# Kernel tuning notes

Hardware: AMD Instinct MI355X
Metric: run time of the kernel (lower is better)

The kernel has to match this reference:

```python
import jax, jax.numpy as jnp
import numpy as np

N_HEAD = 16
HEAD_DIM = 64

def setup_inputs() -> dict:
    key = jax.random.key(0)
    k1, k2, k3 = jax.random.split(key, 3)
    B, S, D = 4, 2048, 1024
    x = jax.random.normal(k1, (B, S, D), dtype=jnp.float32)
    mask = jnp.tril(jnp.ones((S, S), dtype=bool))[None, None]  # (1,1,S,S) causal
    w_attn = jax.random.normal(k2, (D, 3 * D), dtype=jnp.float32) * (1.0 / np.sqrt(D))
    b_attn = jnp.zeros((3 * D,), dtype=jnp.float32)
    w_proj = jax.random.normal(k3, (D, D), dtype=jnp.float32) * (1.0 / np.sqrt(D))
    b_proj = jnp.zeros((D,), dtype=jnp.float32)
    return {"x": x, "mask": mask, "w_attn": w_attn, "b_attn": b_attn,
            "w_proj": w_proj, "b_proj": b_proj}

def reference(x, mask, w_attn, b_attn, w_proj, b_proj):
    B, S, D = x.shape
    H, hd = N_HEAD, HEAD_DIM
    qkv = x @ w_attn + b_attn                      # (B,S,3D)
    q, k, v = jnp.split(qkv, 3, axis=-1)
    q = q.reshape(B, S, H, hd).transpose(0, 2, 1, 3)  # (B,H,S,hd)
    k = k.reshape(B, S, H, hd).transpose(0, 2, 1, 3)
    v = v.reshape(B, S, H, hd).transpose(0, 2, 1, 3)
    scores = jnp.einsum('bhqd,bhkd->bhqk', q, k) / jnp.sqrt(jnp.float32(hd))
    scores = jnp.where(mask, scores, jnp.float32(-1e10))
    weights = jax.nn.softmax(scores, axis=-1)      # dropout is identity (deterministic=True)
    attn = jnp.einsum('bhqk,bhkd->bhqd', weights, v)
    attn = attn.transpose(0, 2, 1, 3).reshape(B, S, D)
    return attn @ w_proj + b_proj
```

## Files before the change

### kernel.cpp

```cpp
#include <hip/hip_runtime.h>
#include <hip/hip_bf16.h>
#include <stdint.h>


typedef uint16_t u16;
typedef __bf16 bf16x8 __attribute__((ext_vector_type(8)));
typedef __bf16 bf16x4 __attribute__((ext_vector_type(4)));
typedef short s16x4 __attribute__((ext_vector_type(4)));
typedef float f32x4 __attribute__((ext_vector_type(4)));

#define S_LEN 2048
#define DMODEL 1024
#define NHEAD 16
#define HDIM 64
#define MTOT 8192
#define NQKV 3072

__device__ __forceinline__ u16 f2bf(float f) {
    union { float f; uint32_t u; } v; v.f = f;
    uint32_t u = v.u;
    return (u16)((u + 0x7fffu + ((u >> 16) & 1u)) >> 16);
}

__device__ __forceinline__ s16x4 bits4(bf16x4 v) {
    union { bf16x4 b; s16x4 s; } u; u.b = v; return u.s;
}

__device__ __forceinline__ f32x4 mfma16(bf16x4 a, bf16x4 b, f32x4 c) {
    return __builtin_amdgcn_mfma_f32_16x16x16bf16_1k(bits4(a), bits4(b), c, 0, 0, 0);
}

__device__ __forceinline__ void async_load16(const void* g, void* l) {
    __builtin_amdgcn_global_load_lds(
        (__attribute__((address_space(1))) void*)g,
        (__attribute__((address_space(3))) void*)l,
        16, 0, 0);
}

__global__ void convert_x_kernel(const float4* __restrict__ in, ushort4* __restrict__ out, int n4) {
    int i = blockIdx.x * 256 + threadIdx.x;
    if (i < n4) {
        float4 f = in[i];
        ushort4 o;
        o.x = f2bf(f.x); o.y = f2bf(f.y); o.z = f2bf(f.z); o.w = f2bf(f.w);
        out[i] = o;
    }
}

__global__ void transpose_bf16_kernel(const float* __restrict__ in, u16* __restrict__ out, int R, int C) {
    __shared__ float tile[64][65];
    int r0 = blockIdx.y * 64, c0 = blockIdx.x * 64;
    #pragma unroll
    for (int i = 0; i < 16; ++i) {
        int idx = threadIdx.x + i * 256;
        int r = idx >> 6, c = idx & 63;
        tile[r][c] = in[(size_t)(r0 + r) * C + c0 + c];
    }
    __syncthreads();
    #pragma unroll
    for (int i = 0; i < 16; ++i) {
        int idx = threadIdx.x + i * 256;
        int c = idx >> 6, r = idx & 63;
        out[(size_t)(c0 + c) * R + r0 + r] = f2bf(tile[r][c]);
    }
}

__global__ void transpose_v_kernel(const u16* __restrict__ qkv, u16* __restrict__ vt) {
    __shared__ u16 tile[64 * 66];
    const int tid = threadIdx.x;
    const int stile = blockIdx.x, bh = blockIdx.y;
    const int b = bh >> 4, h = bh & 15;
    const u16* src = qkv + ((size_t)b * S_LEN + stile * 64) * NQKV + 2 * DMODEL + h * HDIM;
    #pragma unroll
    for (int it = 0; it < 2; ++it) {
        int item = it * 256 + tid;
        int s = item >> 3, d0 = (item & 7) * 8;
        bf16x8 v = *(const bf16x8*)(src + (size_t)s * NQKV + d0);
        const u16* vu = (const u16*)&v;
        #pragma unroll
        for (int j = 0; j < 8; ++j) tile[(d0 + j) * 66 + s] = vu[j];
    }
    __syncthreads();
    #pragma unroll
    for (int it = 0; it < 2; ++it) {
        int item = it * 256 + tid;
        int d = item >> 3, s0 = (item & 7) * 8;
        union { u16 u[8]; uint4 v; } pk;
        #pragma unroll
        for (int j = 0; j < 8; ++j) pk.u[j] = tile[d * 66 + s0 + j];
        *(uint4*)(vt + ((size_t)bh * 64 + d) * S_LEN + stile * 64 + s0) = pk.v;
    }
}

template<int NF, bool OUT_BF16>
__global__ __launch_bounds__(512, 2) void gemm16q(
    const u16* __restrict__ A, const u16* __restrict__ Bt,
    const float* __restrict__ bias, void* __restrict__ C,
    int M, int N, int K)
{
    constexpr int NBH = NF / 2;
    constexpr int BSLOT = NF * 4096;
    __shared__ __attribute__((aligned(16))) u16 sm[32768 + 2 * BSLOT];
    u16* const As = sm;
    u16* const Bs = sm + 32768;

    const int tid = threadIdx.x;
    const int wave = tid >> 6, lane = tid & 63;
    const int l15 = lane & 15, q4 = lane >> 4;
    const int wm = wave >> 2, wn = wave & 3;

    const int bid = (int)blockIdx.x;
    const int xcd = bid & 7;
    const int lx  = bid >> 3;
    const int MB  = M >> 8;
    const int PM  = MB >> 3;
    const int nb  = lx / PM;
    const int mb  = xcd * PM + (lx - nb * PM);
    const int m0 = mb << 8, n0 = nb * NF * 64;

    const u16* Ag = A + (size_t)m0 * K;
    const u16* Bg = Bt + (size_t)n0 * K;

    const int srow = tid >> 3;
    const size_t goff0 = (size_t)srow * K + (size_t)(((tid & 7) ^ (srow & 7)) * 8);
    const size_t goff1 = goff0 + (size_t)64 * K;
    const int ldso = tid * 8;

    const int ck0 = (q4 ^ (l15 & 7)) * 8;
    const int ck1 = ((4 + q4) ^ (l15 & 7)) * 8;
    const int rb0 = (wn * NF * 16 + l15) * 64;

    f32x4 acc[8][NF] = {};
    const int T = K >> 6;

#define STAGE_A(t_, h_) do { \
    const u16* ga_ = Ag + (size_t)(h_) * 128 * K + (size_t)(t_) * 64; \
    u16* da_ = As + (((t_) & 1) * 2 + (h_)) * 8192; \
    async_load16(ga_ + goff0, da_ + ldso); \
    async_load16(ga_ + goff1, da_ + ldso + 4096); \
} while (0)

#define STAGE_B(t_, h_) do { \
    const u16* gb_ = Bg + (size_t)(h_) * 128 * K + (size_t)(t_) * 64; \
    u16* db_ = Bs + ((t_) & 1) * BSLOT + (h_) * 8192; \
    async_load16(gb_ + goff0, db_ + ldso); \
    async_load16(gb_ + goff1, db_ + ldso + 4096); \
} while (0)

#define LOAD_AF(P_) do { \
    af[0][0] = *(const bf16x8*)(Ah + ((2 * (P_)) * 16 + l15) * 64 + ck0); \
    af[0][1] = *(const bf16x8*)(Ah + ((2 * (P_)) * 16 + l15) * 64 + ck1); \
    af[1][0] = *(const bf16x8*)(Ah + ((2 * (P_) + 1) * 16 + l15) * 64 + ck0); \
    af[1][1] = *(const bf16x8*)(Ah + ((2 * (P_) + 1) * 16 + l15) * 64 + ck1); \
} while (0)

#define PHASE_MFMA(P_) do { \
    __builtin_amdgcn_s_barrier(); \
    __builtin_amdgcn_s_setprio(1); \
    _Pragma("unroll") \
    for (int i_ = 0; i_ < 2; ++i_) \
        _Pragma("unroll") \
        for (int nf_ = 0; nf_ < NF; ++nf_) \
            _Pragma("unroll") \
            for (int kk_ = 0; kk_ < 2; ++kk_) \
                acc[2 * (P_) + i_][nf_] = __builtin_amdgcn_mfma_f32_16x16x32_bf16( \
                    af[i_][kk_], bfr[nf_][kk_], acc[2 * (P_) + i_][nf_], 0, 0, 0); \
    __builtin_amdgcn_s_setprio(0); \
} while (0)

    STAGE_A(0, 0); STAGE_A(0, 1);
    STAGE_B(0, 0); if constexpr (NBH == 2) STAGE_B(0, 1);
    if (T > 1) {
        STAGE_B(1, 0); if constexpr (NBH == 2) STAGE_B(1, 1);
        if constexpr (NBH == 2) asm volatile("s_waitcnt vmcnt(4)");
        else                    asm volatile("s_waitcnt vmcnt(2)");
    } else {
        asm volatile("s_waitcnt vmcnt(0)");
    }
    __builtin_amdgcn_sched_barrier(0);
    __builtin_amdgcn_s_barrier();

    for (int t = 0; t < T; ++t) {
        const int par = t & 1;
        const u16* Ah = As + (par * 2 + wm) * 8192;
        const u16* Bl = Bs + par * BSLOT;

        bf16x8 af[2][2], bfr[NF][2];

        #pragma unroll
        for (int nf = 0; nf < NF; ++nf) {
            bfr[nf][0] = *(const bf16x8*)(Bl + rb0 + nf * (16 * 64) + ck0);
            bfr[nf][1] = *(const bf16x8*)(Bl + rb0 + nf * (16 * 64) + ck1);
        }
        LOAD_AF(0);
        if (t + 1 < T) STAGE_A(t + 1, 0);
        PHASE_MFMA(0);
        __builtin_amdgcn_s_barrier();

        LOAD_AF(1);
        if (t + 1 < T) STAGE_A(t + 1, 1);
        PHASE_MFMA(1);
        __builtin_amdgcn_s_barrier();

        LOAD_AF(2);
        if (t + 2 < T) STAGE_B(t + 2, 0);
        PHASE_MFMA(2);
        __builtin_amdgcn_s_barrier();

        LOAD_AF(3);
        if constexpr (NBH == 2) { if (t + 2 < T) STAGE_B(t + 2, 1); }
        PHASE_MFMA(3);
        if (t + 1 < T) {
            if (t + 2 < T) {
                if constexpr (NBH == 2) asm volatile("s_waitcnt vmcnt(4)");
                else                    asm volatile("s_waitcnt vmcnt(2)");
            } else {
                asm volatile("s_waitcnt vmcnt(0)");
            }
            __builtin_amdgcn_sched_barrier(0);
            __builtin_amdgcn_s_barrier();
        }
    }

#undef STAGE_A
#undef STAGE_B
#undef LOAD_AF
#undef PHASE_MFMA

    #pragma unroll
    for (int mf = 0; mf < 8; ++mf) {
        const int row = m0 + wm * 128 + mf * 16 + q4 * 4;
        #pragma unroll
        for (int nf = 0; nf < NF; ++nf) {
            const int col = n0 + wn * NF * 16 + nf * 16 + l15;
            const float bv = bias[col];
            #pragma unroll
            for (int r = 0; r < 4; ++r) {
                float v = acc[mf][nf][r] + bv;
                if (OUT_BF16) ((u16*)C)[(size_t)(row + r) * N + col] = f2bf(v);
                else          ((float*)C)[(size_t)(row + r) * N + col] = v;
            }
        }
    }
}

__device__ __forceinline__ void stage_tiles(
    const u16* __restrict__ qkv, const u16* __restrict__ vt,
    size_t base, int bh, int h, int w, int srow8, int schunk,
    int kt, u16* __restrict__ KsB, u16* __restrict__ VsB)
{
    #pragma unroll
    for (int q = 0; q < 2; ++q) {
        int rloc = w * 16 + q * 8 + srow8;
        int sc = ((schunk ^ (rloc & 7)) * 8);
        async_load16(qkv + (base + (size_t)kt * 64 + rloc) * (size_t)NQKV + DMODEL + h * HDIM + sc,
                     KsB + (w * 16 + q * 8) * 64);
        async_load16(vt + ((size_t)bh * 64 + rloc) * S_LEN + kt * 64 + sc,
                     VsB + (w * 16 + q * 8) * 64);
    }
}

__device__ __forceinline__ void attn_pass(
    int qt, const u16* __restrict__ qkv, const u16* __restrict__ vt,
    __bf16* __restrict__ outb, u16 (*Ks)[64 * 64], u16 (*Vs)[64 * 64],
    int w, int lane, int bh, int h, size_t base)
{
    const int l15 = lane & 15, q4 = lane >> 4;
    const int srow8 = lane >> 3, schunk = lane & 7;

    const float QSCALE = 0.125f * 1.44269504f;
    bf16x8 qf[2][2];
    #pragma unroll
    for (int mh = 0; mh < 2; ++mh) {
        int qrow = qt * 128 + mh * 64 + w * 16 + l15;
        #pragma unroll
        for (int kc = 0; kc < 2; ++kc) {
            bf16x8 raw = *(const bf16x8*)(qkv + (base + qrow) * (size_t)NQKV + h * HDIM + kc * 32 + q4 * 8);
            bf16x8 sc;
            #pragma unroll
            for (int j = 0; j < 8; ++j) sc[j] = (__bf16)((float)raw[j] * QSCALE);
            qf[mh][kc] = sc;
        }
    }

    bf16x4 ones4;
    #pragma unroll
    for (int j = 0; j < 4; ++j) ones4[j] = (__bf16)1.0f;

    f32x4 o0[4] = {}, o1[4] = {};
    f32x4 la0 = {}, la1 = {};

    const int ktlast = 2 * qt + 1;

    __syncthreads();
    stage_tiles(qkv, vt, base, bh, h, w, srow8, schunk, 0, Ks[0], Vs[0]);
    if (ktlast >= 1)
        stage_tiles(qkv, vt, base, bh, h, w, srow8, schunk, 1, Ks[1], Vs[1]);

    for (int kt = 0; kt <= 2 * qt; ++kt) {
        const int buf = kt % 3;
        __syncthreads();
        int pf = kt + 2;
        if (pf <= ktlast)
            stage_tiles(qkv, vt, base, bh, h, w, srow8, schunk, pf, Ks[pf % 3], Vs[pf % 3]);

        f32x4 st0[4] = {}, st1[4] = {};
        #pragma unroll
        for (int nt = 0; nt < 4; ++nt) {
            int n = nt * 16 + l15;
            #pragma unroll
            for (int kc = 0; kc < 2; ++kc) {
                int ch = (((kc * 4 + q4) ^ (n & 7)) * 8);
                bf16x8 kf = *(const bf16x8*)(&Ks[buf][n * 64 + ch]);
                st0[nt] = __builtin_amdgcn_mfma_f32_16x16x32_bf16(kf, qf[0][kc], st0[nt], 0, 0, 0);
                st1[nt] = __builtin_amdgcn_mfma_f32_16x16x32_bf16(kf, qf[1][kc], st1[nt], 0, 0, 0);
            }
        }

        if (kt == 2 * qt) {
            #pragma unroll
            for (int nt = 0; nt < 4; ++nt)
                #pragma unroll
                for (int r = 0; r < 4; ++r) {
                    int keyl = nt * 16 + q4 * 4 + r;
                    if (keyl > w * 16 + l15) st0[nt][r] = -1e30f;
                }
        }

        bf16x4 pb0[4], pb1[4];
        #pragma unroll
        for (int nt = 0; nt < 4; ++nt)
            #pragma unroll
            for (int r = 0; r < 4; ++r) {
                pb0[nt][r] = (__bf16)__builtin_amdgcn_exp2f(st0[nt][r]);
                pb1[nt][r] = (__bf16)__builtin_amdgcn_exp2f(st1[nt][r]);
            }

        #pragma unroll
        for (int nt = 0; nt < 4; ++nt) {
            #pragma unroll
            for (int mt = 0; mt < 4; ++mt) {
                int row = mt * 16 + l15;
                int ch = (nt * 2 + (q4 >> 1)) ^ (row & 7);
                bf16x4 vf = *(const bf16x4*)(&Vs[buf][row * 64 + ch * 8 + (q4 & 1) * 4]);
                o0[mt] = mfma16(vf, pb0[nt], o0[mt]);
                o1[mt] = mfma16(vf, pb1[nt], o1[mt]);
            }
            la0 = mfma16(ones4, pb0[nt], la0);
            la1 = mfma16(ones4, pb1[nt], la1);
        }
    }

    {
        const int buf = ktlast % 3;
        __syncthreads();

        f32x4 st1[4] = {};
        #pragma unroll
        for (int nt = 0; nt < 4; ++nt) {
            int n = nt * 16 + l15;
            #pragma unroll
            for (int kc = 0; kc < 2; ++kc) {
                int ch = (((kc * 4 + q4) ^ (n & 7)) * 8);
                bf16x8 kf = *(const bf16x8*)(&Ks[buf][n * 64 + ch]);
                st1[nt] = __builtin_amdgcn_mfma_f32_16x16x32_bf16(kf, qf[1][kc], st1[nt], 0, 0, 0);
            }
        }
        bf16x4 pb1[4];
        #pragma unroll
        for (int nt = 0; nt < 4; ++nt)
            #pragma unroll
            for (int r = 0; r < 4; ++r) {
                int keyl = nt * 16 + q4 * 4 + r;
                float s = (keyl > w * 16 + l15) ? -1e30f : st1[nt][r];
                pb1[nt][r] = (__bf16)__builtin_amdgcn_exp2f(s);
            }
        #pragma unroll
        for (int nt = 0; nt < 4; ++nt) {
            #pragma unroll
            for (int mt = 0; mt < 4; ++mt) {
                int row = mt * 16 + l15;
                int ch = (nt * 2 + (q4 >> 1)) ^ (row & 7);
                bf16x4 vf = *(const bf16x4*)(&Vs[buf][row * 64 + ch * 8 + (q4 & 1) * 4]);
                o1[mt] = mfma16(vf, pb1[nt], o1[mt]);
            }
            la1 = mfma16(ones4, pb1[nt], la1);
        }
    }

    float inv0 = 1.0f / la0[0], inv1 = 1.0f / la1[0];
    int row0 = qt * 128 + w * 16 + l15;
    int row1 = row0 + 64;
    #pragma unroll
    for (int mt = 0; mt < 4; ++mt) {
        union { __bf16 b[4]; ushort4 v; } p0, p1;
        #pragma unroll
        for (int r = 0; r < 4; ++r) {
            p0.b[r] = (__bf16)(o0[mt][r] * inv0);
            p1.b[r] = (__bf16)(o1[mt][r] * inv1);
        }
        int col = h * HDIM + mt * 16 + q4 * 4;
        *(ushort4*)(&outb[(base + row0) * (size_t)DMODEL + col]) = p0.v;
        *(ushort4*)(&outb[(base + row1) * (size_t)DMODEL + col]) = p1.v;
    }
}

__global__ __launch_bounds__(256, 3) void attn_kernel(
    const u16* __restrict__ qkv, const u16* __restrict__ vt, u16* __restrict__ out)
{
    __shared__ __attribute__((aligned(16))) u16 Ks[3][64 * 64];
    __shared__ __attribute__((aligned(16))) u16 Vs[3][64 * 64];

    const int tid = threadIdx.x;
    const int w = tid >> 6, lane = tid & 63;
    const int bh = blockIdx.y;
    const int b = bh >> 4, h = bh & 15;
    const size_t base = (size_t)b * S_LEN;
    const int NT = (int)gridDim.x * 2;

    attn_pass(NT - 1 - (int)blockIdx.x, qkv, vt, (__bf16*)out, Ks, Vs, w, lane, bh, h, base);
    attn_pass((int)blockIdx.x,          qkv, vt, (__bf16*)out, Ks, Vs, w, lane, bh, h, base);
}

extern "C" void kernel_launch(void* const* d_in, const int* in_sizes, int n_in,
                              void* d_out, int out_size, void* d_ws, size_t ws_size,
                              hipStream_t stream) {
    const float* x      = (const float*)d_in[0];
    const float* w_attn = (const float*)d_in[2];
    const float* b_attn = (const float*)d_in[3];
    const float* w_proj = (const float*)d_in[4];
    const float* b_proj = (const float*)d_in[5];

    u16* xb   = (u16*)d_ws;
    u16* wat  = xb  + (size_t)MTOT * DMODEL;
    u16* wpt  = wat + (size_t)NQKV * DMODEL;
    u16* qkv  = wpt + (size_t)DMODEL * DMODEL;
    u16* attn = qkv + (size_t)MTOT * NQKV;
    u16* vt   = xb;

    convert_x_kernel<<<(MTOT * DMODEL / 4 + 255) / 256, 256, 0, stream>>>(
        (const float4*)x, (ushort4*)xb, MTOT * DMODEL / 4);
    transpose_bf16_kernel<<<dim3(NQKV / 64, DMODEL / 64), 256, 0, stream>>>(w_attn, wat, DMODEL, NQKV);
    transpose_bf16_kernel<<<dim3(DMODEL / 64, DMODEL / 64), 256, 0, stream>>>(w_proj, wpt, DMODEL, DMODEL);

    gemm16q<4, true><<<dim3((MTOT / 256) * (NQKV / 256)), 512, 0, stream>>>(
        xb, wat, b_attn, (void*)qkv, MTOT, NQKV, DMODEL);

    transpose_v_kernel<<<dim3(S_LEN / 64, 4 * NHEAD), 256, 0, stream>>>(qkv, vt);

    attn_kernel<<<dim3(S_LEN / 256, 4 * NHEAD), 256, 0, stream>>>(qkv, vt, attn);

    gemm16q<2, false><<<dim3((MTOT / 256) * (DMODEL / 128)), 512, 0, stream>>>(
        attn, wpt, b_proj, d_out, MTOT, DMODEL, DMODEL);
}
```

Measured before the change: 270.0 us.

## Widen attention query tile to 256 rows per pass for K/V reuse

Each attention pass now handles four 64-row query groups (256 rows) instead of two, so every staged K/V tile feeds up to four query groups of MFMAs. Causal masking is applied per group on its diagonal tile, and groups past their diagonal are skipped. The separate tail block is folded into the main loop. The grid halves and launch bounds drop to one block per SM hint. This costs much higher register pressure, fewer blocks, and worse causal load balance in exchange for less K/V staging traffic.

```diff
diff --git a/kernel.cpp b/kernel.cpp
--- a/kernel.cpp
+++ b/kernel.cpp
@@ -269,17 +269,17 @@
     const int srow8 = lane >> 3, schunk = lane & 7;
 
     const float QSCALE = 0.125f * 1.44269504f;
-    bf16x8 qf[2][2];
-    #pragma unroll
-    for (int mh = 0; mh < 2; ++mh) {
-        int qrow = qt * 128 + mh * 64 + w * 16 + l15;
+    bf16x8 qf[4][2];
+    #pragma unroll
+    for (int g = 0; g < 4; ++g) {
+        int qrow = qt * 256 + g * 64 + w * 16 + l15;
         #pragma unroll
         for (int kc = 0; kc < 2; ++kc) {
             bf16x8 raw = *(const bf16x8*)(qkv + (base + qrow) * (size_t)NQKV + h * HDIM + kc * 32 + q4 * 8);
             bf16x8 sc;
             #pragma unroll
             for (int j = 0; j < 8; ++j) sc[j] = (__bf16)((float)raw[j] * QSCALE);
-            qf[mh][kc] = sc;
+            qf[g][kc] = sc;
         }
     }
 
@@ -287,24 +287,23 @@
     #pragma unroll
     for (int j = 0; j < 4; ++j) ones4[j] = (__bf16)1.0f;
 
-    f32x4 o0[4] = {}, o1[4] = {};
-    f32x4 la0 = {}, la1 = {};
-
-    const int ktlast = 2 * qt + 1;
+    f32x4 o[4][4] = {};
+    f32x4 la[4] = {};
+
+    const int ktlast = 4 * qt + 3;
 
     __syncthreads();
     stage_tiles(qkv, vt, base, bh, h, w, srow8, schunk, 0, Ks[0], Vs[0]);
-    if (ktlast >= 1)
-        stage_tiles(qkv, vt, base, bh, h, w, srow8, schunk, 1, Ks[1], Vs[1]);
-
-    for (int kt = 0; kt <= 2 * qt; ++kt) {
+    stage_tiles(qkv, vt, base, bh, h, w, srow8, schunk, 1, Ks[1], Vs[1]);
+
+    for (int kt = 0; kt <= ktlast; ++kt) {
         const int buf = kt % 3;
         __syncthreads();
         int pf = kt + 2;
         if (pf <= ktlast)
             stage_tiles(qkv, vt, base, bh, h, w, srow8, schunk, pf, Ks[pf % 3], Vs[pf % 3]);
 
-        f32x4 st0[4] = {}, st1[4] = {};
+        f32x4 st[4][4] = {};
         #pragma unroll
         for (int nt = 0; nt < 4; ++nt) {
             int n = nt * 16 + l15;
@@ -312,29 +311,31 @@
             for (int kc = 0; kc < 2; ++kc) {
                 int ch = (((kc * 4 + q4) ^ (n & 7)) * 8);
                 bf16x8 kf = *(const bf16x8*)(&Ks[buf][n * 64 + ch]);
-                st0[nt] = __builtin_amdgcn_mfma_f32_16x16x32_bf16(kf, qf[0][kc], st0[nt], 0, 0, 0);
-                st1[nt] = __builtin_amdgcn_mfma_f32_16x16x32_bf16(kf, qf[1][kc], st1[nt], 0, 0, 0);
+                #pragma unroll
+                for (int g = 0; g < 4; ++g)
+                    if (kt <= 4 * qt + g)
+                        st[g][nt] = __builtin_amdgcn_mfma_f32_16x16x32_bf16(
+                            kf, qf[g][kc], st[g][nt], 0, 0, 0);
             }
         }
 
-        if (kt == 2 * qt) {
+        bf16x4 pb[4][4];
+        #pragma unroll
+        for (int g = 0; g < 4; ++g) {
+            if (kt > 4 * qt + g) continue;
+            const bool diag = (kt == 4 * qt + g);
             #pragma unroll
             for (int nt = 0; nt < 4; ++nt)
                 #pragma unroll
                 for (int r = 0; r < 4; ++r) {
-                    int keyl = nt * 16 + q4 * 4 + r;
-                    if (keyl > w * 16 + l15) st0[nt][r] = -1e30f;
+                    float s = st[g][nt][r];
+                    if (diag) {
+                        int keyl = nt * 16 + q4 * 4 + r;
+                        if (keyl > w * 16 + l15) s = -1e30f;
+                    }
+                    pb[g][nt][r] = (__bf16)__builtin_amdgcn_exp2f(s);
                 }
         }
-
-        bf16x4 pb0[4], pb1[4];
-        #pragma unroll
-        for (int nt = 0; nt < 4; ++nt)
-            #pragma unroll
-            for (int r = 0; r < 4; ++r) {
-                pb0[nt][r] = (__bf16)__builtin_amdgcn_exp2f(st0[nt][r]);
-                pb1[nt][r] = (__bf16)__builtin_amdgcn_exp2f(st1[nt][r]);
-            }
 
         #pragma unroll
         for (int nt = 0; nt < 4; ++nt) {
@@ -343,69 +344,35 @@
                 int row = mt * 16 + l15;
                 int ch = (nt * 2 + (q4 >> 1)) ^ (row & 7);
                 bf16x4 vf = *(const bf16x4*)(&Vs[buf][row * 64 + ch * 8 + (q4 & 1) * 4]);
-                o0[mt] = mfma16(vf, pb0[nt], o0[mt]);
-                o1[mt] = mfma16(vf, pb1[nt], o1[mt]);
+                #pragma unroll
+                for (int g = 0; g < 4; ++g)
+                    if (kt <= 4 * qt + g)
+                        o[g][mt] = mfma16(vf, pb[g][nt], o[g][mt]);
             }
-            la0 = mfma16(ones4, pb0[nt], la0);
-            la1 = mfma16(ones4, pb1[nt], la1);
-        }
-    }
-
-    {
-        const int buf = ktlast % 3;
-        __syncthreads();
-
-        f32x4 st1[4] = {};
-        #pragma unroll
-        for (int nt = 0; nt < 4; ++nt) {
-            int n = nt * 16 + l15;
-            #pragma unroll
-            for (int kc = 0; kc < 2; ++kc) {
-                int ch = (((kc * 4 + q4) ^ (n & 7)) * 8);
-                bf16x8 kf = *(const bf16x8*)(&Ks[buf][n * 64 + ch]);
-                st1[nt] = __builtin_amdgcn_mfma_f32_16x16x32_bf16(kf, qf[1][kc], st1[nt], 0, 0, 0);
-            }
-        }
-        bf16x4 pb1[4];
-        #pragma unroll
-        for (int nt = 0; nt < 4; ++nt)
-            #pragma unroll
-            for (int r = 0; r < 4; ++r) {
-                int keyl = nt * 16 + q4 * 4 + r;
-                float s = (keyl > w * 16 + l15) ? -1e30f : st1[nt][r];
-                pb1[nt][r] = (__bf16)__builtin_amdgcn_exp2f(s);
-            }
-        #pragma unroll
-        for (int nt = 0; nt < 4; ++nt) {
-            #pragma unroll
-            for (int mt = 0; mt < 4; ++mt) {
-                int row = mt * 16 + l15;
-                int ch = (nt * 2 + (q4 >> 1)) ^ (row & 7);
-                bf16x4 vf = *(const bf16x4*)(&Vs[buf][row * 64 + ch * 8 + (q4 & 1) * 4]);
-                o1[mt] = mfma16(vf, pb1[nt], o1[mt]);
-            }
-            la1 = mfma16(ones4, pb1[nt], la1);
-        }
-    }
-
-    float inv0 = 1.0f / la0[0], inv1 = 1.0f / la1[0];
-    int row0 = qt * 128 + w * 16 + l15;
-    int row1 = row0 + 64;
-    #pragma unroll
-    for (int mt = 0; mt < 4; ++mt) {
-        union { __bf16 b[4]; ushort4 v; } p0, p1;
-        #pragma unroll
-        for (int r = 0; r < 4; ++r) {
-            p0.b[r] = (__bf16)(o0[mt][r] * inv0);
-            p1.b[r] = (__bf16)(o1[mt][r] * inv1);
-        }
-        int col = h * HDIM + mt * 16 + q4 * 4;
-        *(ushort4*)(&outb[(base + row0) * (size_t)DMODEL + col]) = p0.v;
-        *(ushort4*)(&outb[(base + row1) * (size_t)DMODEL + col]) = p1.v;
-    }
-}
-
-__global__ __launch_bounds__(256, 3) void attn_kernel(
+            #pragma unroll
+            for (int g = 0; g < 4; ++g)
+                if (kt <= 4 * qt + g)
+                    la[g] = mfma16(ones4, pb[g][nt], la[g]);
+        }
+    }
+
+    #pragma unroll
+    for (int g = 0; g < 4; ++g) {
+        float inv = 1.0f / la[g][0];
+        int row = qt * 256 + g * 64 + w * 16 + l15;
+        #pragma unroll
+        for (int mt = 0; mt < 4; ++mt) {
+            union { __bf16 b[4]; ushort4 v; } p;
+            #pragma unroll
+            for (int r = 0; r < 4; ++r)
+                p.b[r] = (__bf16)(o[g][mt][r] * inv);
+            int col = h * HDIM + mt * 16 + q4 * 4;
+            *(ushort4*)(&outb[(base + row) * (size_t)DMODEL + col]) = p.v;
+        }
+    }
+}
+
+__global__ __launch_bounds__(256, 1) void attn_kernel(
     const u16* __restrict__ qkv, const u16* __restrict__ vt, u16* __restrict__ out)
 {
     __shared__ __attribute__((aligned(16))) u16 Ks[3][64 * 64];
@@ -448,7 +415,7 @@
 
     transpose_v_kernel<<<dim3(S_LEN / 64, 4 * NHEAD), 256, 0, stream>>>(qkv, vt);
 
-    attn_kernel<<<dim3(S_LEN / 256, 4 * NHEAD), 256, 0, stream>>>(qkv, vt, attn);
+    attn_kernel<<<dim3(S_LEN / 512, 4 * NHEAD), 256, 0, stream>>>(qkv, vt, attn);
 
     gemm16q<2, false><<<dim3((MTOT / 256) * (DMODEL / 128)), 512, 0, stream>>>(
         attn, wpt, b_proj, d_out, MTOT, DMODEL, DMODEL);
```

Result: slower. 335.3 us (+24.2%).
